# Optimization experiments

Measured on AMD Instinct MI355X. Metric: run time of the kernel, lower is better.

## Reference

```python
import jax, jax.numpy as jnp
import numpy as np


def setup_inputs() -> dict:
    key = jax.random.key(0)
    k0, k1, k2, k3 = jax.random.split(key, 4)
    B, L, D, H = 8, 4096, 300, 128  # batch, leaves (power of 2), embed dim, hidden
    x = jax.random.normal(k0, (B, L, D), jnp.float32)
    W_leaf = jax.random.normal(k1, (D, 2 * H), jnp.float32) * (1.0 / np.sqrt(D))
    b_leaf = jnp.zeros((2 * H,), jnp.float32)
    W_l = jax.random.normal(k2, (H, 5 * H), jnp.float32) * (1.0 / np.sqrt(H))
    W_r = jax.random.normal(k3, (H, 5 * H), jnp.float32) * (1.0 / np.sqrt(H))
    b = jnp.zeros((5 * H,), jnp.float32)
    return {"x": x, "W_leaf": W_leaf, "b_leaf": b_leaf, "W_l": W_l, "W_r": W_r, "b": b}


def reference(x, W_leaf, b_leaf, W_l, W_r, b):
    """Binary TreeLSTM over a complete tree: leaves -> root.

    x: [B, L, D] leaf embeddings, L a power of 2.
    Leaf transform: linear projection split into (h, c) (SPINN-style).
    REDUCE: 5-gate child-sum-of-two composition.
    Returns root hidden state: [B, H].
    """
    H = W_l.shape[0]
    hc = x @ W_leaf + b_leaf                     # [B, L, 2H]
    h, c = hc[..., :H], hc[..., H:]
    levels = int(np.log2(x.shape[1]))
    for _ in range(levels):                      # level-batched tree reduction
        h_l, h_r = h[:, 0::2], h[:, 1::2]        # [B, n/2, H]
        c_l, c_r = c[:, 0::2], c[:, 1::2]
        gates = h_l @ W_l + h_r @ W_r + b        # [B, n/2, 5H]
        i, fl, fr, o, g = jnp.split(gates, 5, axis=-1)
        c = (jax.nn.sigmoid(fl) * c_l
             + jax.nn.sigmoid(fr) * c_r
             + jax.nn.sigmoid(i) * jnp.tanh(g))
        h = jax.nn.sigmoid(o) * jnp.tanh(c)
    return h[:, 0]                               # root hidden state [B, H]
```

## Files before the change

kernel.cpp:

```cpp
#include <hip/hip_runtime.h>
#include <hip/hip_bf16.h>
#include <math.h>


typedef __attribute__((ext_vector_type(8))) short bfrag8;
typedef __attribute__((ext_vector_type(4))) float f32x4;

__device__ __forceinline__ float rcpf(float x) { return __builtin_amdgcn_rcpf(x); }
__device__ __forceinline__ float sigf(float x) { return rcpf(1.0f + __expf(-x)); }
__device__ __forceinline__ float tanh_f(float x) {
    float e = __expf(2.0f * x);
    return 1.0f - 2.0f * rcpf(e + 1.0f);
}
__device__ __forceinline__ short f2bf(float f) {
    __hip_bfloat16 h = __float2bfloat16(&f == nullptr ? 0.0f : f);
    return *reinterpret_cast<short*>(&h);
}
__device__ __forceinline__ bfrag8 pack8(f32x4 a, f32x4 b) {
    union { int i[4]; bfrag8 v; } u;
    asm("v_cvt_pk_bf16_f32 %0, %1, %2" : "=v"(u.i[0]) : "v"(a[0]), "v"(a[1]));
    asm("v_cvt_pk_bf16_f32 %0, %1, %2" : "=v"(u.i[1]) : "v"(a[2]), "v"(a[3]));
    asm("v_cvt_pk_bf16_f32 %0, %1, %2" : "=v"(u.i[2]) : "v"(b[0]), "v"(b[1]));
    asm("v_cvt_pk_bf16_f32 %0, %1, %2" : "=v"(u.i[3]) : "v"(b[2]), "v"(b[3]));
    return u.v;
}
#define GLDS(gp, lp) __builtin_amdgcn_global_load_lds( \
    (const __attribute__((address_space(1))) void*)(gp), \
    (__attribute__((address_space(3))) void*)(lp), 16, 0, 0)

__global__ __launch_bounds__(256) void leaf_kernel(
    const float* __restrict__ x,     const float* __restrict__ Wleaf,
    const float* __restrict__ W_l,   const float* __restrict__ W_r,
    const float* __restrict__ bleaf,
    short* __restrict__ hD,
    float* __restrict__ cD,
    short* __restrict__ Wcat_ch)
{
    __shared__ float Als[128 * 64];
    __shared__ short Bls[8 * 256 * 8];
    const int tid  = threadIdx.x;
    const int w    = tid >> 6, lane = tid & 63;
    const int quad = lane >> 4, l16 = lane & 15;
    const int mBlk = blockIdx.x * 128;
    const int waveM = (w >> 1) * 64, waveN = (w & 1) * 64;

    if (blockIdx.x < 160) {
        #pragma unroll
        for (int e = 0; e < 4; ++e) {
            int idx = blockIdx.x * 1024 + e * 256 + tid;
            int n = idx >> 8, k = idx & 255;
            float v = (k < 128) ? W_l[k * 640 + n] : W_r[(k - 128) * 640 + n];
            Wcat_ch[(((size_t)(k >> 3)) * 640 + n) * 8 + (k & 7)] = f2bf(v);
        }
    }

    f32x4 acc[2][4][4] = {};
    const f32x4 zero4 = {0.f, 0.f, 0.f, 0.f};

    for (int c = 0; c < 5; ++c) {
        const int k0c = c * 64;
        {
            const int q_lds = lane & 15;
            const int rsub  = lane >> 4;
            #pragma unroll
            for (int g = 0; g < 8; ++g) {
                int row = w * 32 + g * 4 + rsub;
                int q_g = (q_lds & 8) | ((q_lds & 7) ^ (row & 7));
                if (c < 4 || q_g < 11) {
                    GLDS(x + (size_t)(mBlk + row) * 300 + k0c + q_g * 4,
                         (char*)Als + (w * 32 + g * 4) * 256);
                } else {
                    *(f32x4*)((char*)Als + row * 256 + q_lds * 16) = zero4;
                }
            }
        }
        #pragma unroll
        for (int uu = 0; uu < 8; ++uu) {
            int ccl = uu, nl = tid;
            int k0  = (c * 8 + ccl) * 8;
            f32x4 v0, v1;
            #pragma unroll
            for (int jj = 0; jj < 4; ++jj)
                v0[jj] = (k0 + jj < 300) ? Wleaf[(size_t)(k0 + jj) * 256 + nl] : 0.0f;
            #pragma unroll
            for (int jj = 0; jj < 4; ++jj)
                v1[jj] = (k0 + 4 + jj < 300) ? Wleaf[(size_t)(k0 + 4 + jj) * 256 + nl] : 0.0f;
            *(bfrag8*)(Bls + (ccl * 256 + nl) * 8) = pack8(v0, v1);
        }
        __syncthreads();
        #pragma unroll
        for (int ks = 0; ks < 2; ++ks) {
            const int ca = ks * 4 + quad;
            bfrag8 af[4];
            #pragma unroll
            for (int i = 0; i < 4; ++i) {
                int r  = waveM + i * 16 + l16;
                int u0 = 2 * ca, u1 = 2 * ca + 1;
                int s0 = (u0 & 8) | ((u0 & 7) ^ (r & 7));
                int s1 = (u1 & 8) | ((u1 & 7) ^ (r & 7));
                f32x4 a0 = *(const f32x4*)(Als + r * 64 + s0 * 4);
                f32x4 a1 = *(const f32x4*)(Als + r * 64 + s1 * 4);
                af[i] = pack8(a0, a1);
            }
            #pragma unroll
            for (int nh = 0; nh < 2; ++nh) {
                bfrag8 bf4[4];
                #pragma unroll
                for (int jn = 0; jn < 4; ++jn)
                    bf4[jn] = *(const bfrag8*)(Bls + (ca * 256 + nh * 128
                                                      + waveN + jn * 16 + l16) * 8);
                #pragma unroll
                for (int i = 0; i < 4; ++i)
                    #pragma unroll
                    for (int jn = 0; jn < 4; ++jn)
                        acc[nh][i][jn] = __builtin_amdgcn_mfma_f32_16x16x32_bf16(
                                             af[i], bf4[jn], acc[nh][i][jn], 0, 0, 0);
            }
        }
        __syncthreads();
    }

    #pragma unroll
    for (int nh = 0; nh < 2; ++nh) {
        #pragma unroll
        for (int i = 0; i < 4; ++i) {
            int row0 = mBlk + waveM + i * 16 + quad * 4;
            #pragma unroll
            for (int jn = 0; jn < 4; ++jn) {
                int col = nh * 128 + waveN + jn * 16 + l16;
                float bv = bleaf[col];
                #pragma unroll
                for (int rg = 0; rg < 4; ++rg) {
                    float v = acc[nh][i][jn][rg] + bv;
                    int m = row0 + rg;
                    if (nh == 0) {
                        int hc = col;
                        hD[(((size_t)((m & 1) * 16 + (hc >> 3))) * 16384 + (m >> 1)) * 8
                           + (hc & 7)] = f2bf(v);
                    } else {
                        cD[(size_t)m * 128 + (col - 128)] = v;
                    }
                }
            }
        }
    }
}

__global__ __launch_bounds__(256, 2) void level_ws_kernel(
    const short* __restrict__ A,
    const float* __restrict__ cprev,
    const short* __restrict__ Wch,
    const float* __restrict__ bias,
    short* __restrict__ hout, float* __restrict__ cout_,
    int M, int nst)
{
    __shared__ short Als[32 * 64 * 8];
    const int tid  = threadIdx.x;
    const int w    = tid >> 6, lane = tid & 63;
    const int quad = lane >> 4, l16 = lane & 15;
    const int j   = blockIdx.y;
    const int tb0 = blockIdx.x * 64 * nst;
    const int h   = j * 16 + l16;

    #pragma unroll
    for (int s = 0; s < 8; ++s)
        GLDS(A + ((size_t)(s * 4 + w) * M + tb0 + lane) * 8,
             (char*)Als + (s * 4 + w) * 1024);

    bfrag8 Wfr[5][8];
    #pragma unroll
    for (int g = 0; g < 5; ++g)
        #pragma unroll
        for (int s = 0; s < 8; ++s)
            Wfr[g][s] = *(const bfrag8*)(Wch + ((size_t)(s * 4 + quad) * 640
                                                + g * 128 + h) * 8);
    const float bi  = bias[h],       bfl = bias[128 + h], bfr_ = bias[256 + h];
    const float bo  = bias[384 + h], bg  = bias[512 + h];

    const int Mn = M >> 1;
    for (int st = 0; st < nst; ++st) {
        const int tb = tb0 + st * 64;
        __syncthreads();

        f32x4 acc[5] = {};
        #pragma unroll
        for (int s = 0; s < 8; ++s) {
            bfrag8 af = *(const bfrag8*)(Als + ((s * 4 + quad) * 64 + w * 16 + l16) * 8);
            #pragma unroll
            for (int g = 0; g < 5; ++g)
                acc[g] = __builtin_amdgcn_mfma_f32_16x16x32_bf16(af, Wfr[g][s], acc[g], 0, 0, 0);
        }

        if (st + 1 < nst) {
            __syncthreads();
            #pragma unroll
            for (int s = 0; s < 8; ++s)
                GLDS(A + ((size_t)(s * 4 + w) * M + tb + 64 + lane) * 8,
                     (char*)Als + (s * 4 + w) * 1024);
        }

        #pragma unroll
        for (int rg = 0; rg < 4; ++rg) {
            int m = tb + w * 16 + quad * 4 + rg;
            float gi  = acc[0][rg] + bi;
            float gfl = acc[1][rg] + bfl;
            float gfr = acc[2][rg] + bfr_;
            float go  = acc[3][rg] + bo;
            float gg  = acc[4][rg] + bg;
            float cl  = cprev[(size_t)(2 * m) * 128 + h];
            float cr  = cprev[(size_t)(2 * m + 1) * 128 + h];
            float cn  = sigf(gfl) * cl + sigf(gfr) * cr + sigf(gi) * tanh_f(gg);
            float hn  = sigf(go) * tanh_f(cn);
            hout[(((size_t)((m & 1) * 16 + (h >> 3))) * Mn + (m >> 1)) * 8
                 + (h & 7)] = f2bf(hn);
            cout_[(size_t)m * 128 + h] = cn;
        }
    }
}

__global__ __launch_bounds__(512) void finish_kernel(
    const short* __restrict__ hin,
    const float* __restrict__ cin,
    const short* __restrict__ Wch, const float* __restrict__ bias,
    float* __restrict__ out)
{
    __shared__ short hP[32 * 64 * 8];
    __shared__ short hQ[32 * 32 * 8];
    __shared__ float cA[128 * 128];
    __shared__ float cB[64 * 128];
    const int tid  = threadIdx.x;
    const int w    = tid >> 6, lane = tid & 63;
    const int quad = lane >> 4, l16 = lane & 15;
    const int h    = w * 16 + l16;

    #pragma unroll
    for (int g = 0; g < 4; ++g)
        GLDS(hin + ((size_t)((g * 8 + w) * 64 + lane)) * 8,
             (char*)hP + ((g * 8 + w) * 64) * 16);
    #pragma unroll
    for (int g = 0; g < 8; ++g)
        GLDS(cin + ((size_t)((g * 8 + w) * 64 + lane)) * 4,
             (char*)cA + ((g * 8 + w) * 64) * 16);

    bfrag8 Wfr[5][8];
    #pragma unroll
    for (int g = 0; g < 5; ++g)
        #pragma unroll
        for (int s = 0; s < 8; ++s)
            Wfr[g][s] = *(const bfrag8*)(Wch + ((size_t)(s * 4 + quad) * 640
                                                + g * 128 + h) * 8);
    const float bi  = bias[h],       bfl = bias[128 + h], bfr_ = bias[256 + h];
    const float bo  = bias[384 + h], bg  = bias[512 + h];

    __syncthreads();

    #pragma unroll
    for (int t = 0; t < 4; ++t) {
        const int Mo = 64 >> t;
        const short* hsrc = (t & 1) ? hQ : hP;
        short* hdst       = (t & 1) ? hP : hQ;
        const float* cread  = (t & 1) ? cB : cA;
        float*       cwrite = (t & 1) ? cA : cB;
        const int nrt = (Mo + 15) >> 4;

        for (int rt = 0; rt < nrt; ++rt) {
            f32x4 acc[5] = {};
            #pragma unroll
            for (int s = 0; s < 8; ++s) {
                bfrag8 af = *(const bfrag8*)(hsrc + ((s * 4 + quad) * Mo
                                                     + rt * 16 + l16) * 8);
                #pragma unroll
                for (int g = 0; g < 5; ++g)
                    acc[g] = __builtin_amdgcn_mfma_f32_16x16x32_bf16(
                                 af, Wfr[g][s], acc[g], 0, 0, 0);
            }
            #pragma unroll
            for (int rg = 0; rg < 4; ++rg) {
                int m = rt * 16 + quad * 4 + rg;
                if (m < Mo) {
                    float gi  = acc[0][rg] + bi;
                    float gfl = acc[1][rg] + bfl;
                    float gfr = acc[2][rg] + bfr_;
                    float go  = acc[3][rg] + bo;
                    float gg  = acc[4][rg] + bg;
                    float cl  = cread[(2 * m) * 128 + h];
                    float cr  = cread[(2 * m + 1) * 128 + h];
                    float cn  = sigf(gfl) * cl + sigf(gfr) * cr + sigf(gi) * tanh_f(gg);
                    float hn  = sigf(go) * tanh_f(cn);
                    if (t == 3) {
                        out[(size_t)m * 128 + h] = hn;
                    } else {
                        hdst[(((m & 1) * 16 + (h >> 3)) * (Mo >> 1) + (m >> 1)) * 8
                             + (h & 7)] = f2bf(hn);
                        cwrite[m * 128 + h] = cn;
                    }
                }
            }
        }
        __syncthreads();
    }
}

extern "C" void kernel_launch(void* const* d_in, const int* in_sizes, int n_in,
                              void* d_out, int out_size, void* d_ws, size_t ws_size,
                              hipStream_t stream)
{
    const float* x      = (const float*)d_in[0];
    const float* W_leaf = (const float*)d_in[1];
    const float* b_leaf = (const float*)d_in[2];
    const float* W_l    = (const float*)d_in[3];
    const float* W_r    = (const float*)d_in[4];
    const float* b      = (const float*)d_in[5];
    float* out = (float*)d_out;

    char* p = (char*)d_ws;
    short* hA    = (short*)p; p += (size_t)32 * 16384 * 16 + 1024;
    short* hB    = (short*)p; p += (size_t)32 * 8192 * 16 + 1024;
    float* c0    = (float*)p; p += (size_t)32768 * 128 * 4;
    float* c1    = (float*)p; p += (size_t)16384 * 128 * 4;
    short* WcatC = (short*)p; p += (size_t)32 * 640 * 16;

    leaf_kernel<<<256, 256, 0, stream>>>(
        x, W_leaf, W_l, W_r, b_leaf, hA, c0, WcatC);

    const short* hin = hA; const float* cin = c0;
    int M = 16384;
    for (int lev = 1; lev <= 8; ++lev) {
        short* ho = (lev & 1) ? hB : hA;
        float* co = (lev & 1) ? c1 : c0;
        int nst = (lev == 1) ? 4 : (lev == 2) ? 2 : 1;
        level_ws_kernel<<<dim3(M / (64 * nst), 8), 256, 0, stream>>>(
            hin, cin, WcatC, b, ho, co, M, nst);
        hin = ho; cin = co;
        M >>= 1;
    }

    finish_kernel<<<1, 512, 0, stream>>>(hA, c0, WcatC, b, out);
}
```

Baseline: 167.4 us.

## Store leaf and first-level cell state in bf16 with channel-blocked layout

The leaf kernel now writes the cell state c as bf16 in a layout blocked by 16 channels, halving its write traffic. The first level reads that bf16 state and writes bf16 output; the second level reads bf16 and writes fp32 again for the later levels. Level 3 now uses two steps per block instead of one. This cuts memory traffic on the largest levels, at the cost of lower precision in the cell state early in the tree.

```diff
diff --git a/kernel.cpp b/kernel.cpp
--- a/kernel.cpp
+++ b/kernel.cpp
@@ -13,8 +13,13 @@
     return 1.0f - 2.0f * rcpf(e + 1.0f);
 }
 __device__ __forceinline__ short f2bf(float f) {
-    __hip_bfloat16 h = __float2bfloat16(&f == nullptr ? 0.0f : f);
+    __hip_bfloat16 h = __float2bfloat16(f);
     return *reinterpret_cast<short*>(&h);
+}
+__device__ __forceinline__ float bf2f(short s) {
+    union { unsigned int u; float f; } v;
+    v.u = ((unsigned int)(unsigned short)s) << 16;
+    return v.f;
 }
 __device__ __forceinline__ bfrag8 pack8(f32x4 a, f32x4 b) {
     union { int i[4]; bfrag8 v; } u;
@@ -33,7 +38,7 @@
     const float* __restrict__ W_l,   const float* __restrict__ W_r,
     const float* __restrict__ bleaf,
     short* __restrict__ hD,
-    float* __restrict__ cD,
+    short* __restrict__ cDb,
     short* __restrict__ Wcat_ch)
 {
     __shared__ float Als[128 * 64];
@@ -138,7 +143,9 @@
                         hD[(((size_t)((m & 1) * 16 + (hc >> 3))) * 16384 + (m >> 1)) * 8
                            + (hc & 7)] = f2bf(v);
                     } else {
-                        cD[(size_t)m * 128 + (col - 128)] = v;
+                        int ch = col - 128;
+                        cDb[(size_t)(ch >> 4) * 32768 * 16 + (size_t)m * 16 + (ch & 15)]
+                            = f2bf(v);
                     }
                 }
             }
@@ -146,12 +153,13 @@
     }
 }
 
-__global__ __launch_bounds__(256, 2) void level_ws_kernel(
+template<int CIN_BF, int COUT_BF>
+__global__ __launch_bounds__(256, 2) void level_ws_t(
     const short* __restrict__ A,
-    const float* __restrict__ cprev,
+    const void*  __restrict__ cprev,
     const short* __restrict__ Wch,
     const float* __restrict__ bias,
-    short* __restrict__ hout, float* __restrict__ cout_,
+    short* __restrict__ hout, void* __restrict__ cout_,
     int M, int nst)
 {
     __shared__ short Als[32 * 64 * 8];
@@ -207,13 +215,28 @@
             float gfr = acc[2][rg] + bfr_;
             float go  = acc[3][rg] + bo;
             float gg  = acc[4][rg] + bg;
-            float cl  = cprev[(size_t)(2 * m) * 128 + h];
-            float cr  = cprev[(size_t)(2 * m + 1) * 128 + h];
+            float cl, cr;
+            if (CIN_BF) {
+                const short* cp = (const short*)cprev;
+                size_t base = (size_t)(h >> 4) * ((size_t)2 * M) * 16
+                              + (size_t)(2 * m) * 16 + (h & 15);
+                cl = bf2f(cp[base]);
+                cr = bf2f(cp[base + 16]);
+            } else {
+                const float* cp = (const float*)cprev;
+                cl = cp[(size_t)(2 * m) * 128 + h];
+                cr = cp[(size_t)(2 * m + 1) * 128 + h];
+            }
             float cn  = sigf(gfl) * cl + sigf(gfr) * cr + sigf(gi) * tanh_f(gg);
             float hn  = sigf(go) * tanh_f(cn);
             hout[(((size_t)((m & 1) * 16 + (h >> 3))) * Mn + (m >> 1)) * 8
                  + (h & 7)] = f2bf(hn);
-            cout_[(size_t)m * 128 + h] = cn;
+            if (COUT_BF) {
+                ((short*)cout_)[(size_t)(h >> 4) * (size_t)M * 16
+                                + (size_t)m * 16 + (h & 15)] = f2bf(cn);
+            } else {
+                ((float*)cout_)[(size_t)m * 128 + h] = cn;
+            }
         }
     }
 }
@@ -316,24 +339,29 @@
     char* p = (char*)d_ws;
     short* hA    = (short*)p; p += (size_t)32 * 16384 * 16 + 1024;
     short* hB    = (short*)p; p += (size_t)32 * 8192 * 16 + 1024;
-    float* c0    = (float*)p; p += (size_t)32768 * 128 * 4;
-    float* c1    = (float*)p; p += (size_t)16384 * 128 * 4;
+    char*  c0    = p;         p += (size_t)32768 * 128 * 4;
+    char*  c1    = p;         p += (size_t)16384 * 128 * 4;
     short* WcatC = (short*)p; p += (size_t)32 * 640 * 16;
 
     leaf_kernel<<<256, 256, 0, stream>>>(
-        x, W_leaf, W_l, W_r, b_leaf, hA, c0, WcatC);
-
-    const short* hin = hA; const float* cin = c0;
-    int M = 16384;
-    for (int lev = 1; lev <= 8; ++lev) {
+        x, W_leaf, W_l, W_r, b_leaf, hA, (short*)c0, WcatC);
+
+    level_ws_t<1, 1><<<dim3(16384 / 256, 8), 256, 0, stream>>>(
+        hA, c0, WcatC, b, hB, c1, 16384, 4);
+    level_ws_t<1, 0><<<dim3(8192 / 128, 8), 256, 0, stream>>>(
+        hB, c1, WcatC, b, hA, c0, 8192, 2);
+
+    const short* hin = hA; const char* cin = c0;
+    int M = 4096;
+    for (int lev = 3; lev <= 8; ++lev) {
         short* ho = (lev & 1) ? hB : hA;
-        float* co = (lev & 1) ? c1 : c0;
-        int nst = (lev == 1) ? 4 : (lev == 2) ? 2 : 1;
-        level_ws_kernel<<<dim3(M / (64 * nst), 8), 256, 0, stream>>>(
+        char*  co = (lev & 1) ? c1 : c0;
+        int nst = (lev == 3) ? 2 : 1;
+        level_ws_t<0, 0><<<dim3(M / (64 * nst), 8), 256, 0, stream>>>(
             hin, cin, WcatC, b, ho, co, M, nst);
         hin = ho; cin = co;
         M >>= 1;
     }
 
-    finish_kernel<<<1, 512, 0, stream>>>(hA, c0, WcatC, b, out);
-}
+    finish_kernel<<<1, 512, 0, stream>>>(hA, (const float*)c0, WcatC, b, out);
+}
```

Result: no change. 167.3 us (-0.1%).
